# Kernel optimization log

Measured on AMD Instinct MI355X. Metric: run time of the kernel, lower is better.

The kernel has to match this reference:

```python
import jax, jax.numpy as jnp
import numpy as np

B, L, H, D = 16, 4096, 16, 64
HID = H * D


def setup_inputs() -> dict:
    key = jax.random.key(0)
    ks = jax.random.split(key, 10)
    w = lambda k: jax.random.normal(k, (HID, HID), jnp.float32) * 0.02
    return dict(
        hidden_states=jax.random.normal(ks[0], (B, 1, HID), jnp.float32),
        past_key=jax.random.normal(ks[1], (B, H, L, D), jnp.float32),
        past_value=jax.random.normal(ks[2], (B, H, L, D), jnp.float32),
        attention_mask=jnp.ones((B, L), jnp.float32),
        cache_position=jax.random.randint(ks[3], (B, 1), 0, L, jnp.int32),
        Wq=w(ks[4]), bq=jnp.zeros((HID,), jnp.float32),
        Wk=w(ks[5]), bk=jnp.zeros((HID,), jnp.float32),
        Wv=w(ks[6]), bv=jnp.zeros((HID,), jnp.float32),
        Wo=w(ks[7]), bo=jnp.zeros((HID,), jnp.float32),
    )


def reference(hidden_states, past_key, past_value, attention_mask, cache_position,
              Wq, bq, Wk, bk, Wv, bv, Wo, bo):
    # projections: [B,1,HID]; torch Linear => x @ W.T + b
    q = hidden_states @ Wq.T + bq
    k = hidden_states @ Wk.T + bk
    v = hidden_states @ Wv.T + bv
    # [B,H,1,D]
    q = q.reshape(B, 1, H, D).transpose(0, 2, 1, 3)
    k_new = k.reshape(B, H, D)
    v_new = v.reshape(B, H, D)
    pos = cache_position[:, 0]  # [B]
    bidx = jnp.arange(B)
    # write new token K/V into cache at cache_position (per-batch)
    k_cache = past_key.at[bidx, :, pos].set(k_new)
    v_cache = past_value.at[bidx, :, pos].set(v_new)
    scale = jnp.float32(1.0) / jnp.sqrt(jnp.float32(D))
    scores = jnp.einsum('bhqd,bhkd->bhqk', q, k_cache) * scale  # [B,H,1,L]
    neg = jnp.finfo(scores.dtype).min
    scores = jnp.where(attention_mask[:, None, None, :] > 0, scores, neg)
    p = jax.nn.softmax(scores, axis=-1)
    ctx = jnp.einsum('bhqk,bhkd->bhqd', p, v_cache)  # [B,H,1,D]
    attn_output = ctx.transpose(0, 2, 1, 3).reshape(B, 1, HID) @ Wo.T + bo
    return attn_output, k_cache, v_cache
```

## Files before the change

kernel.cpp:

```cpp
#include <hip/hip_runtime.h>
#include <hip/hip_bf16.h>

#define BATCH 16
#define SEQL  4096
#define NH    16
#define HD    64
#define HID   1024
#define KV_ELEMS (BATCH * NH * SEQL * HD)
#define C2 0.1803368801f

#define NBLK  2048
#define NTILE 65536
#define TPB   (NTILE / NBLK)

#define NCHUNK 8
#define CHUNK  512
#define PSTRIDE 68

typedef float f4 __attribute__((ext_vector_type(4)));

__global__ __launch_bounds__(256) void gemv3(
    const float* __restrict__ x,
    const float* __restrict__ W0, const float* __restrict__ W1,
    const float* __restrict__ W2,
    const float* __restrict__ b0, const float* __restrict__ b1,
    const float* __restrict__ b2,
    float* __restrict__ out)
{
    __shared__ float xs[BATCH * HID];
    const int t = threadIdx.x;
    {
        const f4* src = (const f4*)x;
        f4* dst = (f4*)xs;
        #pragma unroll
        for (int i = 0; i < (BATCH * HID / 4) / 256; ++i)
            dst[t + i * 256] = src[t + i * 256];
    }
    __syncthreads();

    const int which = blockIdx.x >> 8;
    const int ob    = (blockIdx.x & 255) << 2;
    const float* W    = (which == 0) ? W0 : ((which == 1) ? W1 : W2);
    const float* bias = (which == 0) ? b0 : ((which == 1) ? b1 : b2);
    const int col = t >> 6, lane = t & 63;
    const int o = ob + col;
    const float* wrow = W + (size_t)o * HID;

    float acc[BATCH];
    #pragma unroll
    for (int b = 0; b < BATCH; ++b) acc[b] = 0.f;

    #pragma unroll
    for (int i = 0; i < 4; ++i) {
        const int k = (lane << 2) + (i << 8);
        const f4 w4 = *(const f4*)&wrow[k];
        #pragma unroll
        for (int b = 0; b < BATCH; ++b) {
            const f4 h4 = *(const f4*)&xs[b * HID + k];
            acc[b] += w4.x * h4.x + w4.y * h4.y + w4.z * h4.z + w4.w * h4.w;
        }
    }

    #pragma unroll
    for (int b = 0; b < BATCH; ++b) {
        #pragma unroll
        for (int sh = 1; sh < 64; sh <<= 1)
            acc[b] += __shfl_xor(acc[b], sh);
    }
    if (lane == 0) {
        const float bb = bias[o];
        #pragma unroll
        for (int b = 0; b < BATCH; ++b)
            out[which * (BATCH * HID) + b * HID + o] = acc[b] + bb;
    }
}

__global__ __launch_bounds__(256, 8) void attn_sweep(
    const float* __restrict__ qkv,
    const float* __restrict__ past_k,
    const float* __restrict__ past_v,
    const float* __restrict__ mask,
    float* __restrict__ kout,
    float* __restrict__ vout,
    float* __restrict__ Aws,
    float* __restrict__ Lws)
{
    const int blk = blockIdx.x;
    const int t   = threadIdx.x;
    const int g   = t >> 4;
    const int j   = t & 15;
    const int w   = t >> 6;

    __shared__ float sw[4][64];
    __shared__ float slw[4];

    int tile = blk;
    size_t off = (size_t)tile * 1024 + (t << 2);
    f4 k0 = __builtin_nontemporal_load((const f4*)(past_k + off));
    f4 v0 = __builtin_nontemporal_load((const f4*)(past_v + off));
    f4 q0 = *(const f4*)&qkv[(tile >> 8) * HD + (j << 2)];
    float am0 = mask[((tile >> 12) << 12) + ((tile & 255) << 4) + g];

    #pragma unroll 1
    for (int tau = 0; tau < TPB; ++tau) {
        const size_t coff = off;
        const int ctile = tile;
        const f4 kc = k0, vc = v0, qc = q0;
        const float amc = am0;

        if (tau < TPB - 1) {
            tile += NBLK;
            off = (size_t)tile * 1024 + (t << 2);
            k0 = __builtin_nontemporal_load((const f4*)(past_k + off));
            v0 = __builtin_nontemporal_load((const f4*)(past_v + off));
            q0 = *(const f4*)&qkv[(tile >> 8) * HD + (j << 2)];
            am0 = mask[((tile >> 12) << 12) + ((tile & 255) << 4) + g];
        }

        __builtin_nontemporal_store(kc, (f4*)(kout + coff));
        __builtin_nontemporal_store(vc, (f4*)(vout + coff));

        float d = kc.x * qc.x + kc.y * qc.y + kc.z * qc.z + kc.w * qc.w;
        d += __shfl_xor(d, 1);
        d += __shfl_xor(d, 2);
        d += __shfl_xor(d, 4);
        d += __shfl_xor(d, 8);
        float pe = exp2f(d * C2);
        const float p = (amc > 0.f) ? pe : 0.f;

        f4 c4 = { p * vc.x, p * vc.y, p * vc.z, p * vc.w };
        float pw = p;
        c4.x += __shfl_xor(c4.x, 16);  c4.x += __shfl_xor(c4.x, 32);
        c4.y += __shfl_xor(c4.y, 16);  c4.y += __shfl_xor(c4.y, 32);
        c4.z += __shfl_xor(c4.z, 16);  c4.z += __shfl_xor(c4.z, 32);
        c4.w += __shfl_xor(c4.w, 16);  c4.w += __shfl_xor(c4.w, 32);
        pw  += __shfl_xor(pw, 16);     pw  += __shfl_xor(pw, 32);

        if (((t >> 4) & 3) == 0) *(f4*)&sw[w][j << 2] = c4;
        if ((t & 63) == 0) slw[w] = pw;
        __syncthreads();

        if (t < 64) {
            const float A = sw[0][t] + sw[1][t] + sw[2][t] + sw[3][t];
            Aws[((size_t)ctile << 6) + t] = A;
            if (t == 0)
                Lws[ctile] = slw[0] + slw[1] + slw[2] + slw[3];
        }
        __syncthreads();
    }
}

__global__ __launch_bounds__(64) void merge2(
    const float* __restrict__ qkv,
    const float* __restrict__ past_k,
    const float* __restrict__ past_v,
    const float* __restrict__ mask,
    const int*   __restrict__ cpos,
    float* __restrict__ kout,
    float* __restrict__ vout,
    const float* __restrict__ Aws,
    const float* __restrict__ Lws,
    float* __restrict__ ctx)
{
    const int bh = blockIdx.x;
    const int b = bh >> 4;
    const int t = threadIdx.x;
    const int pos = cpos[b];

    float L = 0.f, A = 0.f;
    const float* Ab = Aws + ((size_t)bh << 14);
    const float* Lb = Lws + bh * 256;
    #pragma unroll 4
    for (int i = 0; i < 256; ++i) {
        A += Ab[(i << 6) + t];
        L += Lb[i];
    }

    const size_t rowoff = (size_t)bh * (SEQL * HD) + (size_t)pos * HD + t;
    const int qo = bh * HD + t;
    const float qd  = qkv[qo];
    const float knd = qkv[BATCH * HID + qo];
    const float vnd = qkv[2 * BATCH * HID + qo];
    const float ksd = past_k[rowoff];
    const float vsd = past_v[rowoff];

    kout[rowoff] = knd;
    vout[rowoff] = vnd;

    float dst = qd * ksd, dnw = qd * knd;
    #pragma unroll
    for (int sh = 1; sh < 64; sh <<= 1) {
        dst += __shfl_xor(dst, sh);
        dnw += __shfl_xor(dnw, sh);
    }
    const float am = mask[b * SEQL + pos];
    float ps = 0.f, pn = 0.f;
    if (am > 0.f) { ps = exp2f(dst * C2); pn = exp2f(dnw * C2); }

    L += pn - ps;
    A += pn * vnd - ps * vsd;
    ctx[bh * HD + t] = A / L;
}

__global__ __launch_bounds__(256, 6) void attn_fused(
    const float* __restrict__ qkv,
    const float* __restrict__ past_k,
    const float* __restrict__ past_v,
    const float* __restrict__ mask,
    float* __restrict__ kout,
    float* __restrict__ vout,
    float* __restrict__ part)
{
    const int bh = blockIdx.x, c = blockIdx.y;
    const int b = bh >> 4, h = bh & 15;
    const int t = threadIdx.x;
    const int g = t >> 4, j = t & 15;

    const f4 q4 = *(const f4*)&qkv[b * HID + h * HD + (j << 2)];
    const size_t base = (size_t)bh * (SEQL * HD);
    const float* __restrict__ pkb = past_k + base;
    const float* __restrict__ pvb = past_v + base;
    float* __restrict__ kob = kout + base;
    float* __restrict__ vob = vout + base;
    const float* __restrict__ mrow = mask + b * SEQL;

    float l = 0.f;
    f4 a4 = {0.f, 0.f, 0.f, 0.f};

    #pragma unroll 1
    for (int s = 0; s < CHUNK / 128; ++s) {
        const int r0 = c * CHUNK + s * 128 + g;
        const int o0 = r0 * HD + (j << 2);

        f4 kx[8];
        float am[8];
        #pragma unroll
        for (int u = 0; u < 8; ++u)
            kx[u] = __builtin_nontemporal_load((const f4*)(pkb + o0 + u * (16 * HD)));
        #pragma unroll
        for (int u = 0; u < 8; ++u)
            am[u] = mrow[r0 + u * 16];
        #pragma unroll
        for (int u = 0; u < 8; ++u)
            __builtin_nontemporal_store(kx[u], (f4*)(kob + o0 + u * (16 * HD)));

        float p[8];
        #pragma unroll
        for (int u = 0; u < 8; ++u) {
            float d = kx[u].x * q4.x + kx[u].y * q4.y
                    + kx[u].z * q4.z + kx[u].w * q4.w;
            d += __shfl_xor(d, 1);
            d += __shfl_xor(d, 2);
            d += __shfl_xor(d, 4);
            d += __shfl_xor(d, 8);
            float pe = exp2f(d * C2);
            p[u] = (am[u] > 0.f) ? pe : 0.f;
            l += p[u];
        }

        f4 vx[8];
        #pragma unroll
        for (int u = 0; u < 8; ++u)
            vx[u] = __builtin_nontemporal_load((const f4*)(pvb + o0 + u * (16 * HD)));
        #pragma unroll
        for (int u = 0; u < 8; ++u)
            __builtin_nontemporal_store(vx[u], (f4*)(vob + o0 + u * (16 * HD)));
        #pragma unroll
        for (int u = 0; u < 8; ++u) {
            a4.x += p[u] * vx[u].x;
            a4.y += p[u] * vx[u].y;
            a4.z += p[u] * vx[u].z;
            a4.w += p[u] * vx[u].w;
        }
    }

    __shared__ float sl_[16];
    __shared__ float sa[16][64];
    if (j == 0) sl_[g] = l;
    *(f4*)&sa[g][(j << 2)] = a4;
    __syncthreads();

    float* pr = part + ((size_t)bh * NCHUNK + c) * PSTRIDE;
    if (t < 64) {
        float A = 0.f;
        #pragma unroll
        for (int gg = 0; gg < 16; ++gg) A += sa[gg][t];
        pr[1 + t] = A;
    } else if (t == 64) {
        float L = 0.f;
        #pragma unroll
        for (int gg = 0; gg < 16; ++gg) L += sl_[gg];
        pr[0] = L;
    }
}

__global__ __launch_bounds__(64) void merge_fix(
    const float* __restrict__ qkv,
    const float* __restrict__ past_k,
    const float* __restrict__ past_v,
    const float* __restrict__ mask,
    const int*   __restrict__ cpos,
    float* __restrict__ kout,
    float* __restrict__ vout,
    const float* __restrict__ part,
    float* __restrict__ ctx)
{
    const int bh = blockIdx.x;
    const int b = bh >> 4;
    const int t = threadIdx.x;
    const int pos = cpos[b];

    const size_t rowoff = (size_t)bh * (SEQL * HD) + (size_t)pos * HD + t;
    const int qo = bh * HD + t;
    const float qd  = qkv[qo];
    const float knd = qkv[BATCH * HID + qo];
    const float vnd = qkv[2 * BATCH * HID + qo];
    const float ksd = past_k[rowoff];
    const float vsd = past_v[rowoff];

    kout[rowoff] = knd;
    vout[rowoff] = vnd;

    float dst = qd * ksd, dnw = qd * knd;
    #pragma unroll
    for (int sh = 1; sh < 64; sh <<= 1) {
        dst += __shfl_xor(dst, sh);
        dnw += __shfl_xor(dnw, sh);
    }
    const float am = mask[b * SEQL + pos];
    float ps = 0.f, pn = 0.f;
    if (am > 0.f) { ps = exp2f(dst * C2); pn = exp2f(dnw * C2); }

    const int cc0 = pos / CHUNK;
    float L = 0.f, A = 0.f;
    #pragma unroll
    for (int cc = 0; cc < NCHUNK; ++cc) {
        const float* pr = part + ((size_t)bh * NCHUNK + cc) * PSTRIDE;
        float Lc = pr[0];
        float Ac = pr[1 + t];
        if (cc == cc0) { Lc += pn - ps; Ac += pn * vnd - ps * vsd; }
        L += Lc;
        A += Ac;
    }
    ctx[bh * HD + t] = A / L;
}

extern "C" void kernel_launch(void* const* d_in, const int* in_sizes, int n_in,
                              void* d_out, int out_size, void* d_ws, size_t ws_size,
                              hipStream_t stream) {
    const float* hs   = (const float*)d_in[0];
    const float* pk   = (const float*)d_in[1];
    const float* pv   = (const float*)d_in[2];
    const float* mask = (const float*)d_in[3];
    const int*   cpos = (const int*)d_in[4];
    const float* Wq   = (const float*)d_in[5];
    const float* bq   = (const float*)d_in[6];
    const float* Wk   = (const float*)d_in[7];
    const float* bk   = (const float*)d_in[8];
    const float* Wv   = (const float*)d_in[9];
    const float* bv   = (const float*)d_in[10];
    const float* Wo   = (const float*)d_in[11];
    const float* bo   = (const float*)d_in[12];

    float* out_attn = (float*)d_out;
    float* kout = out_attn + BATCH * HID;
    float* vout = kout + KV_ELEMS;

    float* ws    = (float*)d_ws;
    float* qkv   = ws;
    float* ctx   = ws + 49152;
    float* apart = ws + 65536;
    float* Lws   = ws + 65536;
    float* Aws   = ws + 131072;

    const size_t need_sweep = (size_t)(131072 + (size_t)NTILE * 64) * sizeof(float);
    const bool sweep_ok = ws_size >= need_sweep;

    gemv3<<<dim3(768), 256, 0, stream>>>(hs, Wq, Wk, Wv, bq, bk, bv, qkv);

    if (sweep_ok) {
        attn_sweep<<<dim3(NBLK), 256, 0, stream>>>(qkv, pk, pv, mask,
                                                   kout, vout, Aws, Lws);
        merge2<<<dim3(256), 64, 0, stream>>>(qkv, pk, pv, mask, cpos,
                                             kout, vout, Aws, Lws, ctx);
    } else {
        attn_fused<<<dim3(256, NCHUNK), 256, 0, stream>>>(qkv, pk, pv, mask,
                                                          kout, vout, apart);
        merge_fix<<<dim3(256), 64, 0, stream>>>(qkv, pk, pv, mask, cpos,
                                                kout, vout, apart, ctx);
    }

    gemv3<<<dim3(256), 256, 0, stream>>>(ctx, Wo, Wo, Wo, bo, bo, bo, out_attn);
}
```

Before: 241.0 us.

## Make each wavefront own whole tiles in attention sweep with double-buffered loads

The sweep kernel now gives each wavefront entire 1024-element tiles instead of splitting a tile across the block. This removes the shared-memory reduction and both __syncthreads per tile. Loads for the next tile go into a second register buffer (A/B ping-pong) while the current one is processed, so more memory requests stay in flight per wave. The cost is more registers, with launch bounds lowered from 8 to 5 blocks per CU, which may reduce occupancy.

```diff
diff --git a/kernel.cpp b/kernel.cpp
--- a/kernel.cpp
+++ b/kernel.cpp
@@ -10,14 +10,18 @@
 #define C2 0.1803368801f
 
 #define NBLK  2048
+#define NWV   (NBLK * 4)
 #define NTILE 65536
-#define TPB   (NTILE / NBLK)
+#define TPW   (NTILE / NWV)
 
 #define NCHUNK 8
 #define CHUNK  512
 #define PSTRIDE 68
 
 typedef float f4 __attribute__((ext_vector_type(4)));
+
+#define NT_LOAD(p)    __builtin_nontemporal_load((const f4*)(p))
+#define NT_STORE(v,p) __builtin_nontemporal_store((v), (f4*)(p))
 
 __global__ __launch_bounds__(256) void gemv3(
     const float* __restrict__ x,
@@ -75,7 +79,43 @@
     }
 }
 
-__global__ __launch_bounds__(256, 8) void attn_sweep(
+#define PROCESS(KX, VX, TILE, OFF)                                         \
+  {                                                                        \
+    const int bh_ = (TILE) >> 8;                                           \
+    const int b_  = (TILE) >> 12;                                          \
+    const int sq_ = ((TILE) & 255) << 4;                                   \
+    const f4 q_ = *(const f4*)&qkv[(bh_ << 6) + col4];                     \
+    float l_ = 0.f;                                                        \
+    f4 a_ = {0.f, 0.f, 0.f, 0.f};                                          \
+    _Pragma("unroll")                                                      \
+    for (int u = 0; u < 4; ++u) {                                          \
+      NT_STORE(KX[u], kout + (OFF) + (u << 8) + (lane << 2));              \
+      NT_STORE(VX[u], vout + (OFF) + (u << 8) + (lane << 2));              \
+      const float am_ = mask[(b_ << 12) + sq_ + (u << 2) + grp];           \
+      float d_ = KX[u].x * q_.x + KX[u].y * q_.y                           \
+               + KX[u].z * q_.z + KX[u].w * q_.w;                          \
+      d_ += __shfl_xor(d_, 1);                                             \
+      d_ += __shfl_xor(d_, 2);                                             \
+      d_ += __shfl_xor(d_, 4);                                             \
+      d_ += __shfl_xor(d_, 8);                                             \
+      float pe_ = exp2f(d_ * C2);                                          \
+      const float p_ = (am_ > 0.f) ? pe_ : 0.f;                            \
+      l_ += p_;                                                            \
+      a_.x += p_ * VX[u].x;  a_.y += p_ * VX[u].y;                         \
+      a_.z += p_ * VX[u].z;  a_.w += p_ * VX[u].w;                         \
+    }                                                                      \
+    a_.x += __shfl_xor(a_.x, 16);  a_.x += __shfl_xor(a_.x, 32);           \
+    a_.y += __shfl_xor(a_.y, 16);  a_.y += __shfl_xor(a_.y, 32);           \
+    a_.z += __shfl_xor(a_.z, 16);  a_.z += __shfl_xor(a_.z, 32);           \
+    a_.w += __shfl_xor(a_.w, 16);  a_.w += __shfl_xor(a_.w, 32);           \
+    l_   += __shfl_xor(l_, 16);    l_   += __shfl_xor(l_, 32);             \
+    if (lane < 16)                                                         \
+      *(f4*)&Aws[((size_t)(TILE) << 6) + col4] = a_;                       \
+    else if (lane == 16)                                                   \
+      Lws[TILE] = l_;                                                      \
+  }
+
+__global__ __launch_bounds__(256, 5) void attn_wsweep(
     const float* __restrict__ qkv,
     const float* __restrict__ past_k,
     const float* __restrict__ past_v,
@@ -85,68 +125,45 @@
     float* __restrict__ Aws,
     float* __restrict__ Lws)
 {
-    const int blk = blockIdx.x;
-    const int t   = threadIdx.x;
-    const int g   = t >> 4;
-    const int j   = t & 15;
-    const int w   = t >> 6;
-
-    __shared__ float sw[4][64];
-    __shared__ float slw[4];
-
-    int tile = blk;
-    size_t off = (size_t)tile * 1024 + (t << 2);
-    f4 k0 = __builtin_nontemporal_load((const f4*)(past_k + off));
-    f4 v0 = __builtin_nontemporal_load((const f4*)(past_v + off));
-    f4 q0 = *(const f4*)&qkv[(tile >> 8) * HD + (j << 2)];
-    float am0 = mask[((tile >> 12) << 12) + ((tile & 255) << 4) + g];
-
-    #pragma unroll 1
-    for (int tau = 0; tau < TPB; ++tau) {
-        const size_t coff = off;
-        const int ctile = tile;
-        const f4 kc = k0, vc = v0, qc = q0;
-        const float amc = am0;
-
-        if (tau < TPB - 1) {
-            tile += NBLK;
-            off = (size_t)tile * 1024 + (t << 2);
-            k0 = __builtin_nontemporal_load((const f4*)(past_k + off));
-            v0 = __builtin_nontemporal_load((const f4*)(past_v + off));
-            q0 = *(const f4*)&qkv[(tile >> 8) * HD + (j << 2)];
-            am0 = mask[((tile >> 12) << 12) + ((tile & 255) << 4) + g];
+    const int t    = threadIdx.x;
+    const int lane = t & 63;
+    const int wv   = (blockIdx.x << 2) + (t >> 6);
+    const int grp  = lane >> 4;
+    const int col4 = (lane & 15) << 2;
+
+    f4 kA[4], vA[4], kB[4], vB[4];
+
+    int tileA = wv;
+    size_t oA = (size_t)tileA << 10;
+    #pragma unroll
+    for (int u = 0; u < 4; ++u) {
+        kA[u] = NT_LOAD(past_k + oA + (u << 8) + (lane << 2));
+        vA[u] = NT_LOAD(past_v + oA + (u << 8) + (lane << 2));
+    }
+
+    #pragma unroll
+    for (int kk = 0; kk < TPW / 2; ++kk) {
+        const int tileB = tileA + NWV;
+        const size_t oB = (size_t)tileB << 10;
+        #pragma unroll
+        for (int u = 0; u < 4; ++u) {
+            kB[u] = NT_LOAD(past_k + oB + (u << 8) + (lane << 2));
+            vB[u] = NT_LOAD(past_v + oB + (u << 8) + (lane << 2));
         }
 
-        __builtin_nontemporal_store(kc, (f4*)(kout + coff));
-        __builtin_nontemporal_store(vc, (f4*)(vout + coff));
-
-        float d = kc.x * qc.x + kc.y * qc.y + kc.z * qc.z + kc.w * qc.w;
-        d += __shfl_xor(d, 1);
-        d += __shfl_xor(d, 2);
-        d += __shfl_xor(d, 4);
-        d += __shfl_xor(d, 8);
-        float pe = exp2f(d * C2);
-        const float p = (amc > 0.f) ? pe : 0.f;
-
-        f4 c4 = { p * vc.x, p * vc.y, p * vc.z, p * vc.w };
-        float pw = p;
-        c4.x += __shfl_xor(c4.x, 16);  c4.x += __shfl_xor(c4.x, 32);
-        c4.y += __shfl_xor(c4.y, 16);  c4.y += __shfl_xor(c4.y, 32);
-        c4.z += __shfl_xor(c4.z, 16);  c4.z += __shfl_xor(c4.z, 32);
-        c4.w += __shfl_xor(c4.w, 16);  c4.w += __shfl_xor(c4.w, 32);
-        pw  += __shfl_xor(pw, 16);     pw  += __shfl_xor(pw, 32);
-
-        if (((t >> 4) & 3) == 0) *(f4*)&sw[w][j << 2] = c4;
-        if ((t & 63) == 0) slw[w] = pw;
-        __syncthreads();
-
-        if (t < 64) {
-            const float A = sw[0][t] + sw[1][t] + sw[2][t] + sw[3][t];
-            Aws[((size_t)ctile << 6) + t] = A;
-            if (t == 0)
-                Lws[ctile] = slw[0] + slw[1] + slw[2] + slw[3];
+        PROCESS(kA, vA, tileA, oA);
+
+        if (kk < TPW / 2 - 1) {
+            tileA = tileB + NWV;
+            oA = (size_t)tileA << 10;
+            #pragma unroll
+            for (int u = 0; u < 4; ++u) {
+                kA[u] = NT_LOAD(past_k + oA + (u << 8) + (lane << 2));
+                vA[u] = NT_LOAD(past_v + oA + (u << 8) + (lane << 2));
+            }
         }
-        __syncthreads();
+
+        PROCESS(kB, vB, tileB, oB);
     }
 }
 
@@ -236,13 +253,13 @@
         float am[8];
         #pragma unroll
         for (int u = 0; u < 8; ++u)
-            kx[u] = __builtin_nontemporal_load((const f4*)(pkb + o0 + u * (16 * HD)));
+            kx[u] = NT_LOAD(pkb + o0 + u * (16 * HD));
         #pragma unroll
         for (int u = 0; u < 8; ++u)
             am[u] = mrow[r0 + u * 16];
         #pragma unroll
         for (int u = 0; u < 8; ++u)
-            __builtin_nontemporal_store(kx[u], (f4*)(kob + o0 + u * (16 * HD)));
+            NT_STORE(kx[u], kob + o0 + u * (16 * HD));
 
         float p[8];
         #pragma unroll
@@ -261,10 +278,10 @@
         f4 vx[8];
         #pragma unroll
         for (int u = 0; u < 8; ++u)
-            vx[u] = __builtin_nontemporal_load((const f4*)(pvb + o0 + u * (16 * HD)));
+            vx[u] = NT_LOAD(pvb + o0 + u * (16 * HD));
         #pragma unroll
         for (int u = 0; u < 8; ++u)
-            __builtin_nontemporal_store(vx[u], (f4*)(vob + o0 + u * (16 * HD)));
+            NT_STORE(vx[u], vob + o0 + u * (16 * HD));
         #pragma unroll
         for (int u = 0; u < 8; ++u) {
             a4.x += p[u] * vx[u].x;
@@ -379,8 +396,8 @@
     gemv3<<<dim3(768), 256, 0, stream>>>(hs, Wq, Wk, Wv, bq, bk, bv, qkv);
 
     if (sweep_ok) {
-        attn_sweep<<<dim3(NBLK), 256, 0, stream>>>(qkv, pk, pv, mask,
-                                                   kout, vout, Aws, Lws);
+        attn_wsweep<<<dim3(NBLK), 256, 0, stream>>>(qkv, pk, pv, mask,
+                                                    kout, vout, Aws, Lws);
         merge2<<<dim3(256), 64, 0, stream>>>(qkv, pk, pv, mask, cpos,
                                              kout, vout, Aws, Lws, ctx);
     } else {
```

Result: faster. 223.2 us (-7.4%).
